# Kernel optimization log

Hardware: AMD Instinct MI355X
Metric: run time of the kernel (lower is better)

The kernel has to match this reference:

```python
import jax, jax.numpy as jnp
import numpy as np

DIM = 1024
NUM_HEADS = 16
NUM_GROUPS = 8


def setup_inputs() -> dict:
    key = jax.random.key(0)
    k1, k2, k3, k4 = jax.random.split(key, 4)
    B, L = 4, 4096
    x = jax.random.normal(k1, (B, L, DIM), dtype=jnp.float32)
    # torch Linear weights: [out_features, in_features]
    w_qkv = jax.random.normal(k2, (3 * DIM, DIM), dtype=jnp.float32) * (DIM ** -0.5)
    w_out = jax.random.normal(k3, (DIM, DIM), dtype=jnp.float32) * (DIM ** -0.5)
    b_out = jax.random.normal(k4, (DIM,), dtype=jnp.float32) * 0.01
    return {"x": x, "w_qkv": w_qkv, "w_out": w_out, "b_out": b_out}


def reference(x, w_qkv, w_out, b_out):
    B, L, D = x.shape
    H, G = NUM_HEADS, NUM_GROUPS
    dh = D // H
    lg = L // G  # block length per group
    # fused QKV projection (no bias)
    qkv = x @ w_qkv.T  # [B, L, 3D]
    qkv = qkv.reshape(B, L, 3, H, dh)
    qkv = jnp.transpose(qkv, (2, 0, 3, 1, 4))  # [3, B, H, L, dh]
    q, k, v = qkv[0], qkv[1], qkv[2]
    # group sequence into G blocks of length lg; attention within each block
    q = q.reshape(B, H, G, lg, dh)
    k = k.reshape(B, H, G, lg, dh)
    v = v.reshape(B, H, G, lg, dh)
    scale = dh ** -0.5
    scores = jnp.einsum('bhgld,bhgmd->bhglm', q, k) * scale  # [B,H,G,lg,lg]
    attn = jax.nn.softmax(scores, axis=-1)
    out = jnp.einsum('bhglm,bhgmd->bhgld', attn, v)  # [B,H,G,lg,dh]
    # 'b h g l d -> b (g l) (h d)'
    out = jnp.transpose(out, (0, 2, 3, 1, 4)).reshape(B, L, D)
    return out @ w_out.T + b_out
```

## Files before the change

kernel.cpp:

```cpp
#include <hip/hip_runtime.h>
#include <hip/hip_bf16.h>
#include <stdint.h>

typedef __bf16 bf16_t;
typedef __bf16 bf16x8 __attribute__((ext_vector_type(8)));
typedef float floatx4 __attribute__((ext_vector_type(4)));

#define MFMA_16x16x32_BF16(a, b, c) __builtin_amdgcn_mfma_f32_16x16x32_bf16((a), (b), (c), 0, 0, 0)

__device__ __forceinline__ void gload_lds16(const bf16_t* g, bf16_t* lds_base) {
  __builtin_amdgcn_global_load_lds(
      (const __attribute__((address_space(1))) void*)g,
      (__attribute__((address_space(3))) void*)lds_base, 16, 0, 0);
}

__global__ __launch_bounds__(256)
void f32_to_bf16_kernel(const float* __restrict__ in, bf16_t* __restrict__ out, int n8)
{
  for (int i = blockIdx.x * 256 + threadIdx.x; i < n8; i += gridDim.x * 256) {
    const float* p = in + (size_t)i * 8;
    floatx4 f0 = *(const floatx4*)p;
    floatx4 f1 = *(const floatx4*)(p + 4);
    bf16x8 r;
#pragma unroll
    for (int j = 0; j < 4; j++) { r[j] = (bf16_t)f0[j]; r[j + 4] = (bf16_t)f1[j]; }
    *(bf16x8*)(out + (size_t)i * 8) = r;
  }
}

template <typename TOUT, bool BIAS>
__global__ __launch_bounds__(256)
void gemm_bt(const bf16_t* __restrict__ A, const bf16_t* __restrict__ B,
             const float* __restrict__ bias, TOUT* __restrict__ C,
             int M, int N, int K)
{
  __shared__ bf16_t As[128 * 32];
  __shared__ bf16_t Bs[128 * 32];
  const int t = threadIdx.x;
  const int lane = t & 63;
  const int wave = t >> 6;
  const int quad = lane >> 4, l15 = lane & 15;
  const int wr = wave >> 1, wc = wave & 1;
  const int m0 = blockIdx.y * 128, n0 = blockIdx.x * 128;

  const int c0 = t, c1 = t + 256;
  const bf16_t* ag0 = A + (size_t)(m0 + (c0 >> 2)) * K + (c0 & 3) * 8;
  const bf16_t* ag1 = A + (size_t)(m0 + (c1 >> 2)) * K + (c1 & 3) * 8;
  const bf16_t* bg0 = B + (size_t)(n0 + (c0 >> 2)) * K + (c0 & 3) * 8;
  const bf16_t* bg1 = B + (size_t)(n0 + (c1 >> 2)) * K + (c1 & 3) * 8;
  bf16_t* asd0 = As + (size_t)(wave * 64) * 8;
  bf16_t* asd1 = As + (size_t)(256 + wave * 64) * 8;
  bf16_t* bsd0 = Bs + (size_t)(wave * 64) * 8;
  bf16_t* bsd1 = Bs + (size_t)(256 + wave * 64) * 8;

  floatx4 acc[4][4] = {};

  for (int k0 = 0; k0 < K; k0 += 32) {
    __syncthreads();
    gload_lds16(ag0 + k0, asd0);
    gload_lds16(ag1 + k0, asd1);
    gload_lds16(bg0 + k0, bsd0);
    gload_lds16(bg1 + k0, bsd1);
    __syncthreads();

    bf16x8 af[4], bf[4];
#pragma unroll
    for (int i = 0; i < 4; i++)
      af[i] = *(const bf16x8*)(As + (wr * 64 + i * 16 + l15) * 32 + quad * 8);
#pragma unroll
    for (int i = 0; i < 4; i++)
      bf[i] = *(const bf16x8*)(Bs + (wc * 64 + i * 16 + l15) * 32 + quad * 8);
#pragma unroll
    for (int mi = 0; mi < 4; mi++)
#pragma unroll
      for (int ni = 0; ni < 4; ni++)
        acc[mi][ni] = MFMA_16x16x32_BF16(af[mi], bf[ni], acc[mi][ni]);
  }

#pragma unroll
  for (int ni = 0; ni < 4; ni++) {
    const int col = n0 + wc * 64 + ni * 16 + l15;
    const float bv = BIAS ? bias[col] : 0.0f;
#pragma unroll
    for (int mi = 0; mi < 4; mi++) {
      const size_t rbase = (size_t)(m0 + wr * 64 + mi * 16 + quad * 4) * N + col;
#pragma unroll
      for (int r = 0; r < 4; r++)
        C[rbase + (size_t)r * N] = (TOUT)(acc[mi][ni][r] + bv);
    }
  }
}

__global__ __launch_bounds__(256)
void attn_kernel(const bf16_t* __restrict__ qkv, bf16_t* __restrict__ out)
{
  constexpr int VS = 72;
  __shared__ bf16_t Ks[64 * VS];
  __shared__ bf16_t Vt[64 * VS];
  __shared__ bf16_t Ps[4][16 * VS];

  const int h     = blockIdx.x & 15;
  const int qtile = blockIdx.x >> 4;

  const int t = threadIdx.x;
  const int wave = t >> 6, lane = t & 63;
  const int quad = lane >> 4, l15 = lane & 15;

  const int qrow0 = qtile * 256 + wave * 64;
  const int krow0 = (qtile >> 1) * 512;
  const int qcol = h * 64;
  const int kcol = 1024 + h * 64;
  const int vcol = 2048 + h * 64;

  bf16x8 qf[4][2];
#pragma unroll
  for (int mi = 0; mi < 4; mi++)
#pragma unroll
    for (int kb = 0; kb < 2; kb++)
      qf[mi][kb] = *(const bf16x8*)(qkv + (size_t)(qrow0 + mi * 16 + l15) * 3072 + qcol + kb * 32 + quad * 8);

  floatx4 o[4][4] = {};
  float plsum[4][4] = {};

  const float SCL = 0.125f * 1.44269504088896f;

  const bf16_t* kg0 = qkv + (size_t)(krow0 + (t >> 3)) * 3072 + kcol + (t & 7) * 8;
  const bf16_t* kg1 = qkv + (size_t)(krow0 + 32 + (t >> 3)) * 3072 + kcol + (t & 7) * 8;
  const bf16_t* vg0 = qkv + (size_t)(krow0 + (t & 63)) * 3072 + vcol + (t >> 6) * 8;
  const bf16_t* vg1 = qkv + (size_t)(krow0 + (t & 63)) * 3072 + vcol + ((t >> 6) + 4) * 8;
  bf16_t* ksd0 = Ks + (t >> 3) * VS + (t & 7) * 8;
  bf16_t* ksd1 = Ks + ((t >> 3) + 32) * VS + (t & 7) * 8;
  bf16_t* vtd0 = Vt + (t >> 6) * 8 * VS + (t & 63);
  bf16_t* vtd1 = Vt + ((t >> 6) + 4) * 8 * VS + (t & 63);

  bf16x8 kreg0 = *(const bf16x8*)kg0;
  bf16x8 kreg1 = *(const bf16x8*)kg1;
  bf16x8 vreg0 = *(const bf16x8*)vg0;
  bf16x8 vreg1 = *(const bf16x8*)vg1;

  for (int it = 0; it < 8; it++) {
    __syncthreads();
    *(bf16x8*)ksd0 = kreg0;
    *(bf16x8*)ksd1 = kreg1;
#pragma unroll
    for (int j = 0; j < 8; j++) { vtd0[j * VS] = vreg0[j]; vtd1[j * VS] = vreg1[j]; }
    __syncthreads();

    if (it < 7) {
      const size_t off = (size_t)(it + 1) * 64 * 3072;
      kreg0 = *(const bf16x8*)(kg0 + off);
      kreg1 = *(const bf16x8*)(kg1 + off);
      vreg0 = *(const bf16x8*)(vg0 + off);
      vreg1 = *(const bf16x8*)(vg1 + off);
    }

    bf16x8 kf[4][2], vf[4][2];
#pragma unroll
    for (int ni = 0; ni < 4; ni++)
#pragma unroll
      for (int kb = 0; kb < 2; kb++) {
        kf[ni][kb] = *(const bf16x8*)(Ks + (ni * 16 + l15) * VS + kb * 32 + quad * 8);
        vf[ni][kb] = *(const bf16x8*)(Vt + (ni * 16 + l15) * VS + kb * 32 + quad * 8);
      }

#pragma unroll
    for (int mi = 0; mi < 4; mi++) {
      floatx4 s[4] = {};
      __builtin_amdgcn_s_setprio(1);
#pragma unroll
      for (int ni = 0; ni < 4; ni++) {
        s[ni] = MFMA_16x16x32_BF16(qf[mi][0], kf[ni][0], s[ni]);
        s[ni] = MFMA_16x16x32_BF16(qf[mi][1], kf[ni][1], s[ni]);
      }
      __builtin_amdgcn_s_setprio(0);
#pragma unroll
      for (int r = 0; r < 4; r++) {
        float ps = 0.0f;
#pragma unroll
        for (int ni = 0; ni < 4; ni++) {
          const float p = exp2f(s[ni][r] * SCL);
          ps += p;
          Ps[wave][(quad * 4 + r) * VS + ni * 16 + l15] = (bf16_t)p;
        }
        plsum[mi][r] += ps;
      }
      bf16x8 pf0 = *(const bf16x8*)(Ps[wave] + l15 * VS + quad * 8);
      bf16x8 pf1 = *(const bf16x8*)(Ps[wave] + l15 * VS + 32 + quad * 8);
      __builtin_amdgcn_s_setprio(1);
#pragma unroll
      for (int ni = 0; ni < 4; ni++) {
        o[mi][ni] = MFMA_16x16x32_BF16(pf0, vf[ni][0], o[mi][ni]);
        o[mi][ni] = MFMA_16x16x32_BF16(pf1, vf[ni][1], o[mi][ni]);
      }
      __builtin_amdgcn_s_setprio(0);
    }
  }

#pragma unroll
  for (int mi = 0; mi < 4; mi++)
#pragma unroll
    for (int r = 0; r < 4; r++) {
      float tot = plsum[mi][r];
#pragma unroll
      for (int off = 1; off < 16; off <<= 1)
        tot += __shfl_xor(tot, off, 64);
      const float inv = 1.0f / tot;
      const size_t rbase = (size_t)(qrow0 + mi * 16 + quad * 4 + r) * 1024 + h * 64 + l15;
#pragma unroll
      for (int ni = 0; ni < 4; ni++)
        out[rbase + ni * 16] = (bf16_t)(o[mi][ni][r] * inv);
    }
}

extern "C" void kernel_launch(void* const* d_in, const int* in_sizes, int n_in,
                              void* d_out, int out_size, void* d_ws, size_t ws_size,
                              hipStream_t stream)
{
  const float* x     = (const float*)d_in[0];
  const float* w_qkv = (const float*)d_in[1];
  const float* w_out = (const float*)d_in[2];
  const float* b_out = (const float*)d_in[3];
  float* out = (float*)d_out;

  const size_t WQ = (size_t)3072 * 1024, WO = (size_t)1024 * 1024;
  bf16_t* wq_b = (bf16_t*)d_ws;
  bf16_t* wo_b = wq_b + WQ;

  int rows = 16384;
  while ((size_t)rows * 10240 + (WQ + WO) * 2 > ws_size && rows > 512) rows >>= 1;
  const int nchunk = 16384 / rows;

  bf16_t* qkv_c = wo_b + WO;
  bf16_t* att_c = qkv_c + (size_t)rows * 3072;
  bf16_t* x_c   = att_c + (size_t)rows * 1024;

  f32_to_bf16_kernel<<<1536, 256, 0, stream>>>(w_qkv, wq_b, (int)(WQ / 8));
  f32_to_bf16_kernel<<<512, 256, 0, stream>>>(w_out, wo_b, (int)(WO / 8));

  for (int c = 0; c < nchunk; c++) {
    const float* xc = x + (size_t)c * rows * 1024;
    float* outc = out + (size_t)c * rows * 1024;
    f32_to_bf16_kernel<<<2048, 256, 0, stream>>>(xc, x_c, rows * 128);
    gemm_bt<bf16_t, false><<<dim3(3072 / 128, rows / 128), 256, 0, stream>>>(
        x_c, wq_b, nullptr, qkv_c, rows, 3072, 1024);
    attn_kernel<<<dim3(16 * (rows / 256)), 256, 0, stream>>>(qkv_c, att_c);
    gemm_bt<float, true><<<dim3(1024 / 128, rows / 128), 256, 0, stream>>>(
        att_c, wo_b, b_out, outc, rows, 1024, 1024);
  }
}
```

Baseline: 406.5 us.

## Replace GEMM with 256x256-tile double-buffered swizzled LDS kernel

```diff
diff --git a/kernel.cpp b/kernel.cpp
--- a/kernel.cpp
+++ b/kernel.cpp
@@ -29,61 +29,142 @@
 }
 
 template <typename TOUT, bool BIAS>
-__global__ __launch_bounds__(256)
-void gemm_bt(const bf16_t* __restrict__ A, const bf16_t* __restrict__ B,
-             const float* __restrict__ bias, TOUT* __restrict__ C,
-             int M, int N, int K)
+__global__ __launch_bounds__(512, 1)
+void gemm_bt256(const bf16_t* __restrict__ A, const bf16_t* __restrict__ B,
+                const float* __restrict__ bias, TOUT* __restrict__ C,
+                int M, int N, int K)
 {
-  __shared__ bf16_t As[128 * 32];
-  __shared__ bf16_t Bs[128 * 32];
+  __shared__ bf16_t S[65536];
   const int t = threadIdx.x;
-  const int lane = t & 63;
-  const int wave = t >> 6;
+  const int lane = t & 63, wave = t >> 6;
   const int quad = lane >> 4, l15 = lane & 15;
-  const int wr = wave >> 1, wc = wave & 1;
-  const int m0 = blockIdx.y * 128, n0 = blockIdx.x * 128;
-
-  const int c0 = t, c1 = t + 256;
-  const bf16_t* ag0 = A + (size_t)(m0 + (c0 >> 2)) * K + (c0 & 3) * 8;
-  const bf16_t* ag1 = A + (size_t)(m0 + (c1 >> 2)) * K + (c1 & 3) * 8;
-  const bf16_t* bg0 = B + (size_t)(n0 + (c0 >> 2)) * K + (c0 & 3) * 8;
-  const bf16_t* bg1 = B + (size_t)(n0 + (c1 >> 2)) * K + (c1 & 3) * 8;
-  bf16_t* asd0 = As + (size_t)(wave * 64) * 8;
-  bf16_t* asd1 = As + (size_t)(256 + wave * 64) * 8;
-  bf16_t* bsd0 = Bs + (size_t)(wave * 64) * 8;
-  bf16_t* bsd1 = Bs + (size_t)(256 + wave * 64) * 8;
-
-  floatx4 acc[4][4] = {};
-
-  for (int k0 = 0; k0 < K; k0 += 32) {
-    __syncthreads();
-    gload_lds16(ag0 + k0, asd0);
-    gload_lds16(ag1 + k0, asd1);
-    gload_lds16(bg0 + k0, bsd0);
-    gload_lds16(bg1 + k0, bsd1);
-    __syncthreads();
-
-    bf16x8 af[4], bf[4];
-#pragma unroll
-    for (int i = 0; i < 4; i++)
-      af[i] = *(const bf16x8*)(As + (wr * 64 + i * 16 + l15) * 32 + quad * 8);
-#pragma unroll
-    for (int i = 0; i < 4; i++)
-      bf[i] = *(const bf16x8*)(Bs + (wc * 64 + i * 16 + l15) * 32 + quad * 8);
+  const int wm = wave >> 2, wn = wave & 3;
+
+  const int cpx = gridDim.x >> 3;
+  const int obid = blockIdx.x;
+  const int bid = (obid & 7) * cpx + (obid >> 3);
+  const int nbx = N >> 8;
+  const int bx = bid % nbx, by = bid / nbx;
+  const int m0 = by * 256, n0 = bx * 256;
+
+  uint32_t aoff[4], boff[4];
+  bf16_t* asd[4]; bf16_t* bsd[4];
+#pragma unroll
+  for (int j = 0; j < 4; j++) {
+    const uint32_t o = (uint32_t)(j * 512 + t) * 16u;
+    const uint32_t u = o ^ (((o >> 7) & 7u) << 4);
+    const uint32_t row = u >> 7, colb = u & 127u;
+    aoff[j] = (uint32_t)(m0 + row) * (uint32_t)(K * 2) + colb;
+    boff[j] = (uint32_t)(n0 + row) * (uint32_t)(K * 2) + colb;
+    asd[j] = S + j * 4096 + wave * 512;
+    bsd[j] = S + 32768 + j * 4096 + wave * 512;
+  }
+
+  const uint32_t sw = (uint32_t)((l15 & 7) << 4);
+  const uint32_t ce0 = (((uint32_t)(quad * 16)) ^ sw) >> 1;
+  const uint32_t ce1 = ce0 ^ 32u;
+  const bf16_t* lraA0 = S + (wm * 128 + l15) * 64 + ce0;
+  const bf16_t* lraA1 = S + (wm * 128 + l15) * 64 + ce1;
+  const bf16_t* lraB0 = S + 32768 + (wn * 64 + l15) * 64 + ce0;
+  const bf16_t* lraB1 = S + 32768 + (wn * 64 + l15) * 64 + ce1;
+
+  floatx4 acc[8][4] = {};
+
+  const int NT = K >> 6;
+#pragma unroll
+  for (int j = 0; j < 4; j++) gload_lds16((const bf16_t*)((const char*)A + aoff[j]), asd[j]);
+#pragma unroll
+  for (int j = 0; j < 4; j++) gload_lds16((const bf16_t*)((const char*)B + boff[j]), bsd[j]);
+#pragma unroll
+  for (int j = 0; j < 4; j++) gload_lds16((const bf16_t*)((const char*)A + aoff[j] + 128), asd[j] + 16384);
+#pragma unroll
+  for (int j = 0; j < 4; j++) gload_lds16((const bf16_t*)((const char*)B + boff[j] + 128), bsd[j] + 16384);
+
+  for (int kt = 0; kt < NT; kt++) {
+    const int bo = (kt & 1) * 16384;
+    if (kt < NT - 1) asm volatile("s_waitcnt vmcnt(8)" ::: "memory");
+    else             asm volatile("s_waitcnt vmcnt(0)" ::: "memory");
+    __builtin_amdgcn_s_barrier();
+    __builtin_amdgcn_sched_barrier(0);
+
+    bf16x8 af[4][2], bA[2][2], bB[2][2];
+#pragma unroll
+    for (int mi = 0; mi < 4; mi++) {
+      af[mi][0] = *(const bf16x8*)(lraA0 + bo + mi * 1024);
+      af[mi][1] = *(const bf16x8*)(lraA1 + bo + mi * 1024);
+    }
+#pragma unroll
+    for (int ni = 0; ni < 2; ni++) {
+      bA[ni][0] = *(const bf16x8*)(lraB0 + bo + ni * 1024);
+      bA[ni][1] = *(const bf16x8*)(lraB1 + bo + ni * 1024);
+    }
+    __builtin_amdgcn_s_setprio(1);
 #pragma unroll
     for (int mi = 0; mi < 4; mi++)
 #pragma unroll
-      for (int ni = 0; ni < 4; ni++)
-        acc[mi][ni] = MFMA_16x16x32_BF16(af[mi], bf[ni], acc[mi][ni]);
+      for (int ni = 0; ni < 2; ni++) {
+        acc[mi][ni] = MFMA_16x16x32_BF16(af[mi][0], bA[ni][0], acc[mi][ni]);
+        acc[mi][ni] = MFMA_16x16x32_BF16(af[mi][1], bA[ni][1], acc[mi][ni]);
+      }
+    __builtin_amdgcn_s_setprio(0);
+#pragma unroll
+    for (int ni = 0; ni < 2; ni++) {
+      bB[ni][0] = *(const bf16x8*)(lraB0 + bo + (ni + 2) * 1024);
+      bB[ni][1] = *(const bf16x8*)(lraB1 + bo + (ni + 2) * 1024);
+    }
+    __builtin_amdgcn_s_setprio(1);
+#pragma unroll
+    for (int mi = 0; mi < 4; mi++)
+#pragma unroll
+      for (int ni = 0; ni < 2; ni++) {
+        acc[mi][ni + 2] = MFMA_16x16x32_BF16(af[mi][0], bB[ni][0], acc[mi][ni + 2]);
+        acc[mi][ni + 2] = MFMA_16x16x32_BF16(af[mi][1], bB[ni][1], acc[mi][ni + 2]);
+      }
+    __builtin_amdgcn_s_setprio(0);
+#pragma unroll
+    for (int mi = 0; mi < 4; mi++) {
+      af[mi][0] = *(const bf16x8*)(lraA0 + bo + (mi + 4) * 1024);
+      af[mi][1] = *(const bf16x8*)(lraA1 + bo + (mi + 4) * 1024);
+    }
+    __builtin_amdgcn_s_setprio(1);
+#pragma unroll
+    for (int mi = 0; mi < 4; mi++)
+#pragma unroll
+      for (int ni = 0; ni < 2; ni++) {
+        acc[mi + 4][ni + 2] = MFMA_16x16x32_BF16(af[mi][0], bB[ni][0], acc[mi + 4][ni + 2]);
+        acc[mi + 4][ni + 2] = MFMA_16x16x32_BF16(af[mi][1], bB[ni][1], acc[mi + 4][ni + 2]);
+      }
+    __builtin_amdgcn_s_setprio(0);
+    __builtin_amdgcn_sched_barrier(0);
+    __builtin_amdgcn_s_barrier();
+    __builtin_amdgcn_sched_barrier(0);
+    if (kt + 2 < NT) {
+      const uint32_t kadv = (uint32_t)((kt + 2) * 128);
+#pragma unroll
+      for (int j = 0; j < 4; j++)
+        gload_lds16((const bf16_t*)((const char*)A + aoff[j] + kadv), asd[j] + bo);
+#pragma unroll
+      for (int j = 0; j < 4; j++)
+        gload_lds16((const bf16_t*)((const char*)B + boff[j] + kadv), bsd[j] + bo);
+    }
+    __builtin_amdgcn_s_setprio(1);
+#pragma unroll
+    for (int mi = 0; mi < 4; mi++)
+#pragma unroll
+      for (int ni = 0; ni < 2; ni++) {
+        acc[mi + 4][ni] = MFMA_16x16x32_BF16(af[mi][0], bA[ni][0], acc[mi + 4][ni]);
+        acc[mi + 4][ni] = MFMA_16x16x32_BF16(af[mi][1], bA[ni][1], acc[mi + 4][ni]);
+      }
+    __builtin_amdgcn_s_setprio(0);
   }
 
 #pragma unroll
   for (int ni = 0; ni < 4; ni++) {
-    const int col = n0 + wc * 64 + ni * 16 + l15;
+    const int col = n0 + wn * 64 + ni * 16 + l15;
     const float bv = BIAS ? bias[col] : 0.0f;
 #pragma unroll
-    for (int mi = 0; mi < 4; mi++) {
-      const size_t rbase = (size_t)(m0 + wr * 64 + mi * 16 + quad * 4) * N + col;
+    for (int mi = 0; mi < 8; mi++) {
+      const size_t rbase = (size_t)(m0 + wm * 128 + mi * 16 + quad * 4) * N + col;
 #pragma unroll
       for (int r = 0; r < 4; r++)
         C[rbase + (size_t)r * N] = (TOUT)(acc[mi][ni][r] + bv);
@@ -241,10 +322,10 @@
     const float* xc = x + (size_t)c * rows * 1024;
     float* outc = out + (size_t)c * rows * 1024;
     f32_to_bf16_kernel<<<2048, 256, 0, stream>>>(xc, x_c, rows * 128);
-    gemm_bt<bf16_t, false><<<dim3(3072 / 128, rows / 128), 256, 0, stream>>>(
+    gemm_bt256<bf16_t, false><<<dim3((3072 / 256) * (rows / 256)), 512, 0, stream>>>(
         x_c, wq_b, nullptr, qkv_c, rows, 3072, 1024);
     attn_kernel<<<dim3(16 * (rows / 256)), 256, 0, stream>>>(qkv_c, att_c);
-    gemm_bt<float, true><<<dim3(1024 / 128, rows / 128), 256, 0, stream>>>(
+    gemm_bt256<float, true><<<dim3((1024 / 256) * (rows / 256)), 512, 0, stream>>>(
         att_c, wo_b, b_out, outc, rows, 1024, 1024);
   }
 }
```

Result: faster. 368.7 us (-9.3%).
